# Kernel optimization log

Measured on AMD Instinct MI355X. Metric: run time of the kernel, lower is better.

## Reference

```python
import jax, jax.numpy as jnp
import numpy as np

GROUPS = 32
EPS = 1e-6


def group_norm(x, scale, bias):
    B, C, H, W = x.shape
    xg = x.reshape(B, GROUPS, C // GROUPS, H, W)
    mean = xg.mean(axis=(2, 3, 4), keepdims=True)
    var = xg.var(axis=(2, 3, 4), keepdims=True)
    xg = (xg - mean) * jax.lax.rsqrt(var + EPS)
    x = xg.reshape(B, C, H, W)
    return x * scale[None, :, None, None] + bias[None, :, None, None]


def conv1x1(x, w, b):
    # x: [B,C,H,W], w: [O,C], b: [O]
    return jnp.einsum('bchw,oc->bohw', x, w) + b[None, :, None, None]


def setup_inputs() -> dict:
    key = jax.random.key(0)
    ks = jax.random.split(key, 6)
    B, C, H, W = 8, 256, 64, 64
    s = 1.0 / np.sqrt(C)
    return {
        'x': jax.random.normal(ks[0], (B, C, H, W), dtype=jnp.float32),
        'gn_scale': jnp.ones((C,), dtype=jnp.float32),
        'gn_bias': jnp.zeros((C,), dtype=jnp.float32),
        'wq': jax.random.normal(ks[1], (C, C), dtype=jnp.float32) * s,
        'bq': jnp.zeros((C,), dtype=jnp.float32),
        'wk': jax.random.normal(ks[2], (C, C), dtype=jnp.float32) * s,
        'bk': jnp.zeros((C,), dtype=jnp.float32),
        'wv': jax.random.normal(ks[3], (C, C), dtype=jnp.float32) * s,
        'bv': jnp.zeros((C,), dtype=jnp.float32),
        'wo': jax.random.normal(ks[4], (C, C), dtype=jnp.float32) * s,
        'bo': jnp.zeros((C,), dtype=jnp.float32),
    }


def reference(x, gn_scale, gn_bias, wq, bq, wk, bk, wv, bv, wo, bo):
    skip = x
    h = group_norm(x, gn_scale, gn_bias)
    B, C, H, W = h.shape
    N = H * W
    q = conv1x1(h, wq, bq).reshape(B, C, N)  # [B,C,N]
    k = conv1x1(h, wk, bk).reshape(B, C, N)
    v = conv1x1(h, wv, bv).reshape(B, C, N)
    # scores[b,i,j] = sum_c q[b,c,i] k[b,c,j] / sqrt(C)
    scores = jnp.einsum('bci,bcj->bij', q, k) / jnp.sqrt(jnp.float32(C))
    a = jax.nn.softmax(scores, axis=2)  # softmax over keys j
    # z[b,c,i] = sum_j v[b,c,j] a[b,i,j]
    z = jnp.einsum('bcj,bij->bci', v, a).reshape(B, C, H, W)
    z = conv1x1(z, wo, bo)
    return skip + z
```

## Files before the change

kernel.cpp:

```cpp
#include <hip/hip_runtime.h>
#include <math.h>

typedef __bf16 bf16;
typedef __bf16 bf16x8 __attribute__((ext_vector_type(8)));
typedef __bf16 bf16x4 __attribute__((ext_vector_type(4)));
typedef float  f32x4  __attribute__((ext_vector_type(4)));
typedef float  f32x16 __attribute__((ext_vector_type(16)));
typedef unsigned int u32;
typedef unsigned char u8;
typedef u32 u32x4 __attribute__((ext_vector_type(4)));
typedef int  i32x8 __attribute__((ext_vector_type(8)));

#define MFMA(a, b, c)   __builtin_amdgcn_mfma_f32_16x16x32_bf16((a), (b), (c), 0, 0, 0)
#define MFMAS(a, b, c)                                                           \
  __builtin_amdgcn_mfma_scale_f32_32x32x64_f8f6f4((a), (b), (c), 0, 0,           \
                                                  0, 0x7f7f7f7f, 0, 0x7f7f7f7f)

#define GLOAD_LDS16(g, l)                                                        \
  __builtin_amdgcn_global_load_lds(                                              \
      (const __attribute__((address_space(1))) void*)(g),                        \
      (__attribute__((address_space(3))) void*)(l), 16, 0, 0)

static constexpr int B_ = 8, C_ = 256, N_ = 4096;
static constexpr float QSCALE = 0.09016844005556021f;
static constexpr float PBIAS  = 2.0f;

static constexpr size_t HT_OFF = 0;
static constexpr size_t QT_OFF = 16777216;
static constexpr size_t KT_OFF = 25165824;
static constexpr size_t V_OFF  = 33554432;
static constexpr size_t WQ_OFF = 41943040;
static constexpr size_t WK_OFF = WQ_OFF + 131072;
static constexpr size_t WV_OFF = WK_OFF + 131072;
static constexpr size_t WO_OFF = WV_OFF + 131072;
static constexpr size_t ZN_OFF = WO_OFF + 131072;
static constexpr size_t LS_OFF = ZN_OFF + 33554432;
static constexpr size_t PART_ELEMS = (size_t)B_ * C_ * N_;

__global__ __launch_bounds__(256) void wconv_kernel(
    const float* __restrict__ wq, const float* __restrict__ wk,
    const float* __restrict__ wv, const float* __restrict__ wo,
    bf16* __restrict__ oq, bf16* __restrict__ ok, bf16* __restrict__ ov, bf16* __restrict__ oo) {
  int i = blockIdx.x * 256 + threadIdx.x;
  oq[i] = (bf16)wq[i];
  ok[i] = (bf16)wk[i];
  ov[i] = (bf16)wv[i];
  oo[i] = (bf16)wo[i];
}

__global__ __launch_bounds__(256) void gn_kernel(
    const float* __restrict__ x, const float* __restrict__ gsc, const float* __restrict__ gbi,
    bf16* __restrict__ hT) {
  int b = blockIdx.x >> 5, g = blockIdx.x & 31, c0 = g * 8;
  int t = threadIdx.x;
  const float* base = x + ((size_t)(b * C_ + c0)) * N_;
  float s = 0.f, ss = 0.f;
  const f32x4* b4 = (const f32x4*)base;
#pragma unroll
  for (int p = 0; p < 32; p++) {
    f32x4 v = b4[t + p * 256];
    s  += v[0] + v[1] + v[2] + v[3];
    ss += v[0] * v[0] + v[1] * v[1] + v[2] * v[2] + v[3] * v[3];
  }
#pragma unroll
  for (int off = 1; off < 64; off <<= 1) {
    s  += __shfl_xor(s, off);
    ss += __shfl_xor(ss, off);
  }
  __shared__ float red[8];
  if ((t & 63) == 0) { red[(t >> 6) * 2] = s; red[(t >> 6) * 2 + 1] = ss; }
  __syncthreads();
  s  = red[0] + red[2] + red[4] + red[6];
  ss = red[1] + red[3] + red[5] + red[7];
  float mean = s * (1.f / 32768.f);
  float var  = ss * (1.f / 32768.f) - mean * mean;
  float rstd = rsqrtf(var + 1e-6f);
  float aa[8], bb[8];
#pragma unroll
  for (int cc = 0; cc < 8; cc++) {
    aa[cc] = rstd * gsc[c0 + cc];
    bb[cc] = gbi[c0 + cc] - mean * aa[cc];
  }
  for (int ii = 0; ii < 16; ii++) {
    int i = t + ii * 256;
    bf16x8 o;
#pragma unroll
    for (int cc = 0; cc < 8; cc++) o[cc] = (bf16)(base[(size_t)cc * N_ + i] * aa[cc] + bb[cc]);
    *(bf16x8*)(hT + ((size_t)(b * N_ + i)) * C_ + c0) = o;
  }
}

__global__ __launch_bounds__(256) void qkv_kernel(
    const bf16* __restrict__ hT,
    const bf16* __restrict__ wqb, const bf16* __restrict__ wkb, const bf16* __restrict__ wvb,
    const float* __restrict__ bq, const float* __restrict__ bk, const float* __restrict__ bv,
    u8* __restrict__ qT8, u8* __restrict__ kT8, u8* __restrict__ v8) {
  int b = blockIdx.x >> 6, i0 = (blockIdx.x & 63) << 6;
  int t = threadIdx.x, w = t >> 6, lane = t & 63, quad = lane >> 4, l15 = lane & 15;
  __shared__ bf16 hl[64 * 264];
#pragma unroll
  for (int p = 0; p < 8; p++) {
    int u = t + p * 256, r = u >> 5, c16 = u & 31;
    *(bf16x8*)(hl + r * 264 + c16 * 8) =
        *(const bf16x8*)(hT + ((size_t)(b * N_ + i0 + r)) * C_ + c16 * 8);
  }
  __syncthreads();
  int cw0 = w * 64;

  f32x4 aq[4][4], ak[4][4];
#pragma unroll
  for (int a = 0; a < 4; a++)
#pragma unroll
    for (int bb2 = 0; bb2 < 4; bb2++) { aq[a][bb2] = (f32x4){0.f,0.f,0.f,0.f}; ak[a][bb2] = (f32x4){0.f,0.f,0.f,0.f}; }
  for (int kc = 0; kc < 8; kc++) {
    bf16x8 hb[4];
#pragma unroll
    for (int it = 0; it < 4; it++)
      hb[it] = *(const bf16x8*)(hl + (it * 16 + l15) * 264 + kc * 32 + quad * 8);
#pragma unroll
    for (int ct = 0; ct < 4; ct++) {
      bf16x8 wqf = *(const bf16x8*)(wqb + ((size_t)(cw0 + ct * 16 + l15)) * C_ + kc * 32 + quad * 8);
      bf16x8 wkf = *(const bf16x8*)(wkb + ((size_t)(cw0 + ct * 16 + l15)) * C_ + kc * 32 + quad * 8);
#pragma unroll
      for (int it = 0; it < 4; it++) {
        aq[ct][it] = MFMA(wqf, hb[it], aq[ct][it]);
        ak[ct][it] = MFMA(wkf, hb[it], ak[ct][it]);
      }
    }
  }
#pragma unroll
  for (int ct = 0; ct < 4; ct++)
#pragma unroll
    for (int it = 0; it < 4; it++) {
      int c4 = cw0 + ct * 16 + quad * 4;
      int i  = i0 + it * 16 + l15;
      f32x4 bq4 = *(const f32x4*)(bq + c4);
      f32x4 bk4 = *(const f32x4*)(bk + c4);
      float qv[4], kv[4];
#pragma unroll
      for (int r = 0; r < 4; r++) {
        qv[r] = (aq[ct][it][r] + bq4[r]) * (QSCALE * 4.0f);
        kv[r] = (ak[ct][it][r] + bk4[r]) * 0.25f;
      }
      u32 qd = (u32)__builtin_amdgcn_cvt_pk_fp8_f32(qv[0], qv[1], 0, false);
      qd = (u32)__builtin_amdgcn_cvt_pk_fp8_f32(qv[2], qv[3], (int)qd, true);
      u32 kd = (u32)__builtin_amdgcn_cvt_pk_fp8_f32(kv[0], kv[1], 0, false);
      kd = (u32)__builtin_amdgcn_cvt_pk_fp8_f32(kv[2], kv[3], (int)kd, true);
      *(u32*)(qT8 + ((size_t)(b * N_ + i)) * C_ + c4) = qd;
      *(u32*)(kT8 + ((size_t)(b * N_ + i)) * C_ + c4) = kd;
    }

  f32x4 av[4][4];
#pragma unroll
  for (int a = 0; a < 4; a++)
#pragma unroll
    for (int bb2 = 0; bb2 < 4; bb2++) av[a][bb2] = (f32x4){0.f,0.f,0.f,0.f};
  for (int kc = 0; kc < 8; kc++) {
    bf16x8 ha[4];
#pragma unroll
    for (int it = 0; it < 4; it++)
      ha[it] = *(const bf16x8*)(hl + (it * 16 + l15) * 264 + kc * 32 + quad * 8);
#pragma unroll
    for (int ct = 0; ct < 4; ct++) {
      bf16x8 wvf = *(const bf16x8*)(wvb + ((size_t)(cw0 + ct * 16 + l15)) * C_ + kc * 32 + quad * 8);
#pragma unroll
      for (int it = 0; it < 4; it++) av[it][ct] = MFMA(ha[it], wvf, av[it][ct]);
    }
  }
#pragma unroll
  for (int it = 0; it < 4; it++)
#pragma unroll
    for (int ct = 0; ct < 4; ct++) {
      int c  = cw0 + ct * 16 + l15;
      int i4 = i0 + it * 16 + quad * 4;
      float bvc = bv[c];
      float vv4[4];
#pragma unroll
      for (int r = 0; r < 4; r++) vv4[r] = av[it][ct][r] + bvc;
      u32 vd = (u32)__builtin_amdgcn_cvt_pk_fp8_f32(vv4[0], vv4[1], 0, false);
      vd = (u32)__builtin_amdgcn_cvt_pk_fp8_f32(vv4[2], vv4[3], (int)vd, true);
      *(u32*)(v8 + ((size_t)(b * C_ + c)) * N_ + i4) = vd;
    }
}

__global__ __launch_bounds__(256, 2) void attn_kernel(
    const u8* __restrict__ qT8, const u8* __restrict__ kT8, const u8* __restrict__ v8,
    bf16* __restrict__ zNum, float* __restrict__ lsum) {
  int blk = blockIdx.x;
  int sp = blk >> 8;
  int b = blk & 7;
  int i0 = ((blk >> 3) & 31) << 7;
  int t = threadIdx.x, w = t >> 6, lane = t & 63;
  int r31 = lane & 31, h = lane >> 5;
  __shared__ __align__(16) u8 lds8[16384 + 16384];
  u8* kTl = lds8;
  u8* vl  = lds8 + 16384;

  int iw = i0 + w * 32;
  const u8* qrow = qT8 + ((size_t)(b * N_ + iw + r31)) * C_ + h * 32;
  i32x8 qB[4];
#pragma unroll
  for (int m = 0; m < 4; m++) qB[m] = *(const i32x8*)(qrow + m * 64);

  f32x16 of[8];
#pragma unroll
  for (int ct = 0; ct < 8; ct++)
#pragma unroll
    for (int e = 0; e < 16; e++) of[ct][e] = 0.f;
  float lacc = 0.f;

  int ks = r31 & 7;
  int kr_off = lane >> 4;
  int kc_pos = lane & 15;
  int vr_off = lane >> 2;
  int vc_pos = lane & 3;

  int j0 = sp * 2048;
  for (int jt = 0; jt < 32; jt++, j0 += 64) {
    __syncthreads();
#pragma unroll
    for (int p = 0; p < 4; p++) {
      int idx = w * 4 + p;
      int r = idx * 4 + kr_off;
      int chunk = kc_pos ^ (r & 7);
      GLOAD_LDS16(kT8 + ((size_t)(b * N_ + j0 + r)) * C_ + chunk * 16, kTl + idx * 1024);
    }
#pragma unroll
    for (int p = 0; p < 4; p++) {
      int idx = w * 4 + p;
      int c = idx * 16 + vr_off;
      int chunk = vc_pos ^ ((c >> 1) & 3);
      GLOAD_LDS16(v8 + ((size_t)(b * C_ + c)) * N_ + j0 + chunk * 16, vl + idx * 1024);
    }
    __syncthreads();

    u32 PG0[4], PG1[4];
#pragma unroll
    for (int g = 0; g < 2; g++) {
      f32x16 st;
#pragma unroll
      for (int e = 0; e < 16; e++) st[e] = 0.f;
      const u8* krow = kTl + (g * 32 + r31) * 256;
#pragma unroll
      for (int m = 0; m < 4; m++) {
        int cd = m * 4 + h * 2;
        u32x4 lo = *(const u32x4*)(krow + ((cd ^ ks) * 16));
        u32x4 hi = *(const u32x4*)(krow + (((cd + 1) ^ ks) * 16));
        i32x8 kf;
        kf[0] = lo[0]; kf[1] = lo[1]; kf[2] = lo[2]; kf[3] = lo[3];
        kf[4] = hi[0]; kf[5] = hi[1]; kf[6] = hi[2]; kf[7] = hi[3];
        st = MFMAS(kf, qB[m], st);
      }
#pragma unroll
      for (int b4 = 0; b4 < 4; b4++) {
        float p0 = __builtin_amdgcn_exp2f(st[b4 * 4 + 0] - PBIAS);
        float p1 = __builtin_amdgcn_exp2f(st[b4 * 4 + 1] - PBIAS);
        float p2 = __builtin_amdgcn_exp2f(st[b4 * 4 + 2] - PBIAS);
        float p3 = __builtin_amdgcn_exp2f(st[b4 * 4 + 3] - PBIAS);
        lacc += (p0 + p1) + (p2 + p3);
        u32 d = (u32)__builtin_amdgcn_cvt_pk_fp8_f32(p0, p1, 0, false);
        d = (u32)__builtin_amdgcn_cvt_pk_fp8_f32(p2, p3, (int)d, true);
        if (g == 0) PG0[b4] = d; else PG1[b4] = d;
      }
    }

    u32 A[8];
#pragma unroll
    for (int b4 = 0; b4 < 4; b4++) {
      u32 mine = h ? PG1[b4] : PG0[b4];
      u32 send = h ? PG0[b4] : PG1[b4];
      u32 recv = (u32)__shfl_xor((int)send, 32);
      A[2 * b4]     = h ? recv : mine;
      A[2 * b4 + 1] = h ? mine : recv;
    }
    i32x8 pA;
#pragma unroll
    for (int e = 0; e < 8; e++) pA[e] = (int)A[e];

#pragma unroll
    for (int ct = 0; ct < 8; ct++) {
      int c = ct * 32 + r31;
      int vs = (c >> 1) & 3;
      const u8* vrow = vl + c * 64;
      u32x4 lo = *(const u32x4*)(vrow + (((2 * h) ^ vs) * 16));
      u32x4 hi = *(const u32x4*)(vrow + (((2 * h + 1) ^ vs) * 16));
      i32x8 vB;
      vB[0] = lo[0]; vB[1] = lo[1]; vB[2] = lo[2]; vB[3] = lo[3];
      vB[4] = hi[0]; vB[5] = hi[1]; vB[6] = hi[2]; vB[7] = hi[3];
      of[ct] = MFMAS(pA, vB, of[ct]);
    }
  }

  lacc += __shfl_xor(lacc, 32);
  if (h == 0)
    lsum[((size_t)(sp * 8 + b)) * N_ + iw + r31] = lacc;
  bf16* zn = zNum + (size_t)sp * PART_ELEMS;
#pragma unroll
  for (int ct = 0; ct < 8; ct++) {
    int c = ct * 32 + r31;
#pragma unroll
    for (int g = 0; g < 4; g++) {
      bf16x4 zv;
#pragma unroll
      for (int e = 0; e < 4; e++) zv[e] = (bf16)of[ct][g * 4 + e];
      int i4 = iw + 8 * g + 4 * h;
      *(bf16x4*)(zn + ((size_t)(b * C_ + c)) * N_ + i4) = zv;
    }
  }
}

__global__ __launch_bounds__(256) void combine_kernel(
    const bf16* __restrict__ zNum, const float* __restrict__ lsum,
    const bf16* __restrict__ wob, const float* __restrict__ bo,
    const float* __restrict__ x, float* __restrict__ out) {
  int b = blockIdx.x >> 6, i0 = (blockIdx.x & 63) << 6;
  int t = threadIdx.x, w = t >> 6, lane = t & 63, quad = lane >> 4, l15 = lane & 15;
  __shared__ bf16 zl[64 * 264];
  __shared__ float linv[64];

  if (t < 64) {
    size_t ii = (size_t)b * N_ + i0 + t;
    linv[t] = 1.f / (lsum[ii] + lsum[ii + (size_t)8 * N_]);
  }
  __syncthreads();

#pragma unroll
  for (int p = 0; p < 16; p++) {
    int u = t + p * 256, c = u >> 4, ii = (u & 15) * 4;
    size_t base = ((size_t)(b * C_ + c)) * N_ + i0 + ii;
    bf16x4 z0 = *(const bf16x4*)(zNum + base);
    bf16x4 z1 = *(const bf16x4*)(zNum + PART_ELEMS + base);
#pragma unroll
    for (int e = 0; e < 4; e++)
      zl[(ii + e) * 264 + c] = (bf16)(((float)z0[e] + (float)z1[e]) * linv[ii + e]);
  }
  __syncthreads();

  f32x4 oa[4][4];
#pragma unroll
  for (int a = 0; a < 4; a++)
#pragma unroll
    for (int bb2 = 0; bb2 < 4; bb2++) oa[a][bb2] = (f32x4){0.f, 0.f, 0.f, 0.f};
  for (int kc = 0; kc < 8; kc++) {
    bf16x8 za[4];
#pragma unroll
    for (int it = 0; it < 4; it++)
      za[it] = *(const bf16x8*)(zl + (it * 16 + l15) * 264 + kc * 32 + quad * 8);
#pragma unroll
    for (int ctl = 0; ctl < 4; ctl++) {
      bf16x8 wf = *(const bf16x8*)(wob + ((size_t)(w * 64 + ctl * 16 + l15)) * C_ + kc * 32 + quad * 8);
#pragma unroll
      for (int it = 0; it < 4; it++) oa[ctl][it] = MFMA(za[it], wf, oa[ctl][it]);
    }
  }
#pragma unroll
  for (int ctl = 0; ctl < 4; ctl++)
#pragma unroll
    for (int it = 0; it < 4; it++) {
      int c = w * 64 + ctl * 16 + l15;
      size_t base = ((size_t)(b * C_ + c)) * N_ + i0 + it * 16 + quad * 4;
      f32x4 xs = *(const f32x4*)(x + base);
      float boc = bo[c];
      f32x4 o4;
#pragma unroll
      for (int r = 0; r < 4; r++) o4[r] = oa[ctl][it][r] + boc + xs[r];
      *(f32x4*)(out + base) = o4;
    }
}

extern "C" void kernel_launch(void* const* d_in, const int* in_sizes, int n_in,
                              void* d_out, int out_size, void* d_ws, size_t ws_size,
                              hipStream_t stream) {
  const float* x   = (const float*)d_in[0];
  const float* gsc = (const float*)d_in[1];
  const float* gbi = (const float*)d_in[2];
  const float* wq  = (const float*)d_in[3];
  const float* bq  = (const float*)d_in[4];
  const float* wk  = (const float*)d_in[5];
  const float* bk  = (const float*)d_in[6];
  const float* wv  = (const float*)d_in[7];
  const float* bv  = (const float*)d_in[8];
  const float* wo  = (const float*)d_in[9];
  const float* bo  = (const float*)d_in[10];

  char* ws = (char*)d_ws;
  bf16* hT   = (bf16*)(ws + HT_OFF);
  u8*   qT8  = (u8*)(ws + QT_OFF);
  u8*   kT8  = (u8*)(ws + KT_OFF);
  u8*   v8   = (u8*)(ws + V_OFF);
  bf16* wqb  = (bf16*)(ws + WQ_OFF);
  bf16* wkb  = (bf16*)(ws + WK_OFF);
  bf16* wvb  = (bf16*)(ws + WV_OFF);
  bf16* wob  = (bf16*)(ws + WO_OFF);
  bf16* zNum = (bf16*)(ws + ZN_OFF);
  float* lsum = (float*)(ws + LS_OFF);

  wconv_kernel<<<256, 256, 0, stream>>>(wq, wk, wv, wo, wqb, wkb, wvb, wob);
  gn_kernel<<<256, 256, 0, stream>>>(x, gsc, gbi, hT);
  qkv_kernel<<<512, 256, 0, stream>>>(hT, wqb, wkb, wvb, bq, bk, bv, qT8, kT8, v8);
  attn_kernel<<<512, 256, 0, stream>>>(qT8, kT8, v8, zNum, lsum);
  combine_kernel<<<512, 256, 0, stream>>>(zNum, lsum, wob, bo, x, (float*)d_out);
}
```

Before: 255.1 us.

## Double-buffer K/V tiles in attention and cache x in LDS for group norm

The attention kernel now prefetches the next K/V tile into a second LDS buffer with async global-to-LDS loads while computing on the current one. It waits with a partial vmcnt and raw barriers instead of full syncthreads. Separately, the group-norm kernel uses 512 threads and stages x as bf16 in shared memory during the statistics pass, so the normalize pass no longer rereads x from global memory. The costs are doubled attention LDS (64KB), which may cut occupancy at 2 blocks per CU, and normalizing a bf16-rounded x instead of the fp32 input.

Result: no change. 251.6 us (-1.3%).

```diff
diff --git a/kernel.cpp b/kernel.cpp
--- a/kernel.cpp
+++ b/kernel.cpp
@@ -48,30 +48,37 @@
   oo[i] = (bf16)wo[i];
 }
 
-__global__ __launch_bounds__(256) void gn_kernel(
+__global__ __launch_bounds__(512) void gn_kernel(
     const float* __restrict__ x, const float* __restrict__ gsc, const float* __restrict__ gbi,
     bf16* __restrict__ hT) {
   int b = blockIdx.x >> 5, g = blockIdx.x & 31, c0 = g * 8;
   int t = threadIdx.x;
   const float* base = x + ((size_t)(b * C_ + c0)) * N_;
+  __shared__ bf16 xl[32768];
   float s = 0.f, ss = 0.f;
   const f32x4* b4 = (const f32x4*)base;
 #pragma unroll
-  for (int p = 0; p < 32; p++) {
-    f32x4 v = b4[t + p * 256];
+  for (int p = 0; p < 16; p++) {
+    int u = t + p * 512;
+    f32x4 v = b4[u];
     s  += v[0] + v[1] + v[2] + v[3];
     ss += v[0] * v[0] + v[1] * v[1] + v[2] * v[2] + v[3] * v[3];
+    bf16x4 xv;
+#pragma unroll
+    for (int e = 0; e < 4; e++) xv[e] = (bf16)v[e];
+    *(bf16x4*)(xl + u * 4) = xv;
   }
 #pragma unroll
   for (int off = 1; off < 64; off <<= 1) {
     s  += __shfl_xor(s, off);
     ss += __shfl_xor(ss, off);
   }
-  __shared__ float red[8];
+  __shared__ float red[16];
   if ((t & 63) == 0) { red[(t >> 6) * 2] = s; red[(t >> 6) * 2 + 1] = ss; }
   __syncthreads();
-  s  = red[0] + red[2] + red[4] + red[6];
-  ss = red[1] + red[3] + red[5] + red[7];
+  s = 0.f; ss = 0.f;
+#pragma unroll
+  for (int r = 0; r < 8; r++) { s += red[r * 2]; ss += red[r * 2 + 1]; }
   float mean = s * (1.f / 32768.f);
   float var  = ss * (1.f / 32768.f) - mean * mean;
   float rstd = rsqrtf(var + 1e-6f);
@@ -81,11 +88,12 @@
     aa[cc] = rstd * gsc[c0 + cc];
     bb[cc] = gbi[c0 + cc] - mean * aa[cc];
   }
-  for (int ii = 0; ii < 16; ii++) {
-    int i = t + ii * 256;
+#pragma unroll
+  for (int ii = 0; ii < 8; ii++) {
+    int i = t + ii * 512;
     bf16x8 o;
 #pragma unroll
-    for (int cc = 0; cc < 8; cc++) o[cc] = (bf16)(base[(size_t)cc * N_ + i] * aa[cc] + bb[cc]);
+    for (int cc = 0; cc < 8; cc++) o[cc] = (bf16)((float)xl[cc * 4096 + i] * aa[cc] + bb[cc]);
     *(bf16x8*)(hT + ((size_t)(b * N_ + i)) * C_ + c0) = o;
   }
 }
@@ -192,9 +200,7 @@
   int i0 = ((blk >> 3) & 31) << 7;
   int t = threadIdx.x, w = t >> 6, lane = t & 63;
   int r31 = lane & 31, h = lane >> 5;
-  __shared__ __align__(16) u8 lds8[16384 + 16384];
-  u8* kTl = lds8;
-  u8* vl  = lds8 + 16384;
+  __shared__ __align__(16) u8 lds8[2 * 32768];
 
   int iw = i0 + w * 32;
   const u8* qrow = qT8 + ((size_t)(b * N_ + iw + r31)) * C_ + h * 32;
@@ -215,24 +221,36 @@
   int vr_off = lane >> 2;
   int vc_pos = lane & 3;
 
-  int j0 = sp * 2048;
-  for (int jt = 0; jt < 32; jt++, j0 += 64) {
-    __syncthreads();
+  auto stage = [&](int jts, int buf) {
+    int j0s = sp * 2048 + jts * 64;
+    u8* kb = lds8 + buf * 32768;
+    u8* vb = kb + 16384;
 #pragma unroll
     for (int p = 0; p < 4; p++) {
       int idx = w * 4 + p;
       int r = idx * 4 + kr_off;
       int chunk = kc_pos ^ (r & 7);
-      GLOAD_LDS16(kT8 + ((size_t)(b * N_ + j0 + r)) * C_ + chunk * 16, kTl + idx * 1024);
+      GLOAD_LDS16(kT8 + ((size_t)(b * N_ + j0s + r)) * C_ + chunk * 16, kb + idx * 1024);
     }
 #pragma unroll
     for (int p = 0; p < 4; p++) {
       int idx = w * 4 + p;
       int c = idx * 16 + vr_off;
       int chunk = vc_pos ^ ((c >> 1) & 3);
-      GLOAD_LDS16(v8 + ((size_t)(b * C_ + c)) * N_ + j0 + chunk * 16, vl + idx * 1024);
-    }
-    __syncthreads();
+      GLOAD_LDS16(v8 + ((size_t)(b * C_ + c)) * N_ + j0s + chunk * 16, vb + idx * 1024);
+    }
+  };
+
+  stage(0, 0);
+
+  for (int jt = 0; jt < 32; jt++) {
+    int cur = jt & 1;
+    __builtin_amdgcn_s_barrier();
+    stage(jt < 31 ? jt + 1 : 31, cur ^ 1);
+    asm volatile("s_waitcnt vmcnt(8)" ::: "memory");
+    __builtin_amdgcn_s_barrier();
+    const u8* kTl = lds8 + cur * 32768;
+    const u8* vl  = kTl + 16384;
 
     u32 PG0[4], PG1[4];
 #pragma unroll
@@ -396,7 +414,7 @@
   float* lsum = (float*)(ws + LS_OFF);
 
   wconv_kernel<<<256, 256, 0, stream>>>(wq, wk, wv, wo, wqb, wkb, wvb, wob);
-  gn_kernel<<<256, 256, 0, stream>>>(x, gsc, gbi, hT);
+  gn_kernel<<<256, 512, 0, stream>>>(x, gsc, gbi, hT);
   qkv_kernel<<<512, 256, 0, stream>>>(hT, wqb, wkb, wvb, bq, bk, bv, qT8, kT8, v8);
   attn_kernel<<<512, 256, 0, stream>>>(qT8, kT8, v8, zNum, lsum);
   combine_kernel<<<512, 256, 0, stream>>>(zNum, lsum, wob, bo, x, (float*)d_out);
```
